# Kernel optimization log

Hardware: AMD Instinct MI355X
Metric: run time of the kernel (lower is better)

Reference implementation:

```python
import jax, jax.numpy as jnp
import numpy as np
from jax import lax

B, IC, OC, H, W_DIM, K = 8, 64, 64, 256, 512, 3
BLUR_1D = [1.0, 3.0, 3.0, 1.0]
FACTOR = 2
GAIN = 1.0


def _blur_kernel():
    # setup_resample_kernel: outer product of 1D kernel, normalized to sum 1
    k = np.asarray(BLUR_1D, dtype=np.float32)
    k = np.outer(k, k)
    k = k / np.sum(k)
    return k  # [4,4]


def setup_inputs() -> dict:
    key = jax.random.key(0)
    ks = jax.random.split(key, 5)
    x = jax.random.normal(ks[0], (B, IC, H, H), dtype=jnp.float32)
    w = jax.random.normal(ks[1], (B, W_DIM), dtype=jnp.float32)
    # init_std = 1.0 for both weights since lrmul = 1.0
    w_conv = jax.random.normal(ks[2], (K, K, IC, OC), dtype=jnp.float32)
    w_dense = jax.random.normal(ks[3], (W_DIM, IC), dtype=jnp.float32)
    b_mod = jnp.zeros((IC,), dtype=jnp.float32)
    return {"x": x, "w": w, "w_conv": w_conv, "w_dense": w_dense, "b_mod": b_mod}


def reference(x, w, w_conv, w_dense, b_mod):
    k = w_conv.shape[0]
    ic, oc = w_conv.shape[2], w_conv.shape[3]

    # runtime coefs (equalized lr): he_std = gain / sqrt(fan_in), lrmul = 1
    coef_conv = 1.0 / np.sqrt(k * k * ic)
    coef_dense = 1.0 / np.sqrt(w.shape[1])

    # style = Dense(w) + bias (linear act, gain 1) + 1.0   -> [B, IC]
    style = w @ (coef_dense * w_dense) + b_mod + 1.0

    # modulate: [B,k,k,IC,OC]
    wmod = (coef_conv * w_conv)[None] * style[:, None, None, :, None]
    # demodulate over (kh, kw, ic)
    d = lax.rsqrt(jnp.sum(jnp.square(wmod), axis=(1, 2, 3)) + 1e-8)  # [B,OC]
    wmod = wmod * d[:, None, None, None, :]

    # per-sample grouped transposed conv (upsample x2) == lhs-dilated cross-corr
    # with the unflipped modulated weight, padding k-1 on each side.
    w_oihw = jnp.transpose(wmod, (0, 4, 3, 1, 2))  # [B,OC,IC,k,k]

    def up_conv(xb, wb):
        return lax.conv_general_dilated(
            xb[None], wb, window_strides=(1, 1),
            padding=[(k - 1, k - 1), (k - 1, k - 1)],
            lhs_dilation=(FACTOR, FACTOR),
            dimension_numbers=("NCHW", "OIHW", "NCHW"))[0]

    y = jax.vmap(up_conv)(x, w_oihw)  # [B,OC,(H-1)*2+k,(W-1)*2+k] = [B,OC,513,513]

    # upfirdn blur: kernel scaled by gain * factor**2, pad0 = pad1 = 1,
    # true convolution (kernel flipped in reference) applied depthwise.
    kb = jnp.asarray(_blur_kernel() * (GAIN * FACTOR ** 2))  # [4,4]
    fw = kb[::-1, ::-1][None, None]  # [1,1,4,4]
    b_, c_, s1, s2 = y.shape
    y = lax.conv_general_dilated(
        y.reshape(b_ * c_, 1, s1, s2), fw, window_strides=(1, 1),
        padding=[(1, 1), (1, 1)],
        dimension_numbers=("NCHW", "OIHW", "NCHW"))
    # output spatial: s1 + 2 - 4 + 1 = 2H
    return y.reshape(b_, c_, y.shape[2], y.shape[3])
```

## Files before the change

kernel.cpp:

```cpp
#include <hip/hip_runtime.h>

#define NB 8
#define IC 64
#define OC 64
#define HH 256
#define WD 512
#define PP 258

typedef __bf16 bf16x8 __attribute__((ext_vector_type(8)));
typedef float f32x16 __attribute__((ext_vector_type(16)));
typedef float f32x4 __attribute__((ext_vector_type(4)));

__device__ inline void compute_E(const float* __restrict__ w_conv, float stv,
                                 int oc, float E[6][6]) {
  const float coef_conv = 1.0f / 24.0f;
  const float s = stv * coef_conv;
  const int ic = threadIdx.x & 63;

  float wm[3][3];
  float ssq = 0.f;
  #pragma unroll
  for (int kh = 0; kh < 3; ++kh)
    #pragma unroll
    for (int kw = 0; kw < 3; ++kw) {
      float v = w_conv[((kh * 3 + kw) * IC + ic) * OC + oc] * s;
      wm[kh][kw] = v;
      ssq += v * v;
    }
  #pragma unroll
  for (int off = 32; off > 0; off >>= 1) ssq += __shfl_xor(ssq, off);
  const float d = rsqrtf(ssq + 1e-8f);
  #pragma unroll
  for (int kh = 0; kh < 3; ++kh)
    #pragma unroll
    for (int kw = 0; kw < 3; ++kw) wm[kh][kw] *= d;

  const float g[4] = {0.25f, 0.75f, 0.75f, 0.25f};
  #pragma unroll
  for (int a = 0; a < 6; ++a)
    #pragma unroll
    for (int c = 0; c < 6; ++c) {
      float acc = 0.f;
      #pragma unroll
      for (int dh = 0; dh < 3; ++dh) {
        int u = a - dh;
        if (u < 0 || u > 3) continue;
        #pragma unroll
        for (int dw = 0; dw < 3; ++dw) {
          int v = c - dw;
          if (v < 0 || v > 3) continue;
          acc = fmaf(wm[dh][dw], g[u] * g[v], acc);
        }
      }
      E[a][c] = acc;
    }
}

__device__ inline float style_of(const float* __restrict__ w,
                                 const float* __restrict__ w_dense,
                                 const float* __restrict__ b_mod, int b,
                                 int ic) {
  const float coef_dense = 0.044194173824159216f;
  const float* wr = w + b * WD;
  float acc = 0.f;
  for (int k = 0; k < WD; ++k) acc = fmaf(wr[k], w_dense[k * IC + ic], acc);
  return acc * coef_dense + b_mod[ic] + 1.0f;
}

#define XS 268
__global__ __launch_bounds__(256) void pre_kernel(
    const float* __restrict__ x, const float* __restrict__ w,
    const float* __restrict__ w_dense, const float* __restrict__ b_mod,
    const float* __restrict__ w_conv, __bf16* __restrict__ xTg,
    __bf16* __restrict__ PWf) {
  __shared__ unsigned short buf[64 * XS];
  const int tid = threadIdx.x;
  const int bid = blockIdx.x;

  if (bid >= 2056) {
    const int bid2 = bid - 2056;
    const int b = bid2 >> 4;
    const int ocq = bid2 & 15;
    const int oc = ocq * 4 + (tid >> 6);
    const int ic = tid & 63;

    float stv = style_of(w, w_dense, b_mod, b, ic);
    float E[6][6];
    compute_E(w_conv, stv, oc, E);

    const int ks = ic >> 4;
    const int h = (ic >> 3) & 1;
    const int e = ic & 7;
    const int lane = (oc & 31) + 32 * h;
    const int ocg = oc >> 5;

    #pragma unroll
    for (int pp = 0; pp < 2; ++pp)
      #pragma unroll
      for (int pq = 0; pq < 2; ++pq) {
        const int ph = pp * 2 + pq;
        #pragma unroll
        for (int j = 0; j < 3; ++j)
          #pragma unroll
          for (int l = 0; l < 3; ++l) {
            const int tap = j * 3 + l;
            float val = E[2 * j + 1 - pp][2 * l + 1 - pq];
            size_t off =
                ((size_t)(((((b * 4 + ph) * 9 + tap) * 2 + ocg) * 4 + ks)) *
                     64 + lane) * 8 + e;
            PWf[off] = (__bf16)val;
          }
      }
    return;
  }

  const int m = bid % 257;
  const int b = bid / 257;

  if (m == 256) {
    uint4 z = make_uint4(0, 0, 0, 0);
    for (int i = tid; i < 8224; i += 256) {
      int pix = i >> 3;
      int sub = i & 7;
      int pr, pc;
      if (pix < 258) {
        pr = 0; pc = pix;
      } else if (pix < 516) {
        pr = 257; pc = pix - 258;
      } else {
        int rem = pix - 516;
        pr = 1 + (rem >> 1);
        pc = (rem & 1) ? 257 : 0;
      }
      *(uint4*)(xTg + ((size_t)(b * PP + pr) * PP + pc) * 64 + sub * 8) = z;
    }
    return;
  }

  const int ln = tid & 63, grp = tid >> 6;
  #pragma unroll
  for (int p = 0; p < 16; ++p) {
    const int ic = p * 4 + grp;
    float4 v = *(const float4*)(x + ((size_t)(b * 64 + ic) * 256 + m) * 256 +
                                ln * 4);
    ushort4 u4;
    u4.x = __builtin_bit_cast(unsigned short, (__bf16)v.x);
    u4.y = __builtin_bit_cast(unsigned short, (__bf16)v.y);
    u4.z = __builtin_bit_cast(unsigned short, (__bf16)v.z);
    u4.w = __builtin_bit_cast(unsigned short, (__bf16)v.w);
    *(ushort4*)&buf[ic * XS + ln * 4] = u4;
  }
  __syncthreads();
  #pragma unroll
  for (int it = 0; it < 8; ++it) {
    int pix = it * 32 + (tid >> 3);
    int g = tid & 7;
    bf16x8 o;
    #pragma unroll
    for (int e = 0; e < 8; ++e)
      o[e] = __builtin_bit_cast(__bf16, buf[(g * 8 + e) * XS + pix]);
    *(bf16x8*)(xTg + ((size_t)(b * PP + m + 1) * PP + (pix + 1)) * 64 +
               g * 8) = o;
  }
}

#define GLD_LDS(src, dst)                                                \
  __builtin_amdgcn_global_load_lds(                                      \
      (const __attribute__((address_space(1))) void*)(src),              \
      (__attribute__((address_space(3))) void*)(dst), 16, 0, 0)

__global__ __launch_bounds__(512, 2) void conv32f_kernel(
    const __bf16* __restrict__ xTg, const __bf16* __restrict__ PWf,
    float* __restrict__ out) {
  __shared__ __bf16 band[4 * 130 * 8 * 8];

  const int tid = threadIdx.x;
  const int lane = tid & 63;
  const int wv = tid >> 6;
  const int pq = wv & 1;
  const int pp = (wv >> 1) & 1;
  const int og = wv >> 2;
  const int ln31 = lane & 31;
  const int lh = lane >> 5;

  const int raw = blockIdx.x;
  const int bid = (raw & 7) * 256 + (raw >> 3);
  const int nh = bid & 1;
  const int mt = (bid >> 1) & 127;
  const int b = bid >> 8;
  const int mr = mt * 2;

  const int ph = b * 4 + pp * 2 + pq;
  const bf16x8* Awave =
      (const bf16x8*)PWf + ((size_t)ph * 72 + og * 4) * 64 + lane;

  {
    const int wb = wv * 520;
    #pragma unroll
    for (int it = 0; it < 9; ++it) {
      int o = it * 64 + lane;
      if (o < 520) {
        int L = wb + o;
        int row = L / 1040;
        int rem = L - row * 1040;
        int col = rem >> 3;
        int s = rem & 7;
        int g = s ^ (col & 7);
        const __bf16* src =
            xTg + ((size_t)(b * PP + mr + row) * PP + nh * 128 + col) * 64 +
            g * 8;
        GLD_LDS(src, band + (size_t)L * 8);
      }
    }
  }
  asm volatile("s_waitcnt vmcnt(0)" ::: "memory");
  __builtin_amdgcn_s_barrier();

  f32x16 acc[2][4];
  #pragma unroll
  for (int mw = 0; mw < 2; ++mw)
    #pragma unroll
    for (int ns = 0; ns < 4; ++ns)
      #pragma unroll
      for (int e = 0; e < 16; ++e) acc[mw][ns][e] = 0.f;

  #pragma unroll
  for (int ks = 0; ks < 4; ++ks) {
    #pragma unroll
    for (int l = 0; l < 3; ++l) {
      bf16x8 Ac[3];
      #pragma unroll
      for (int j = 0; j < 3; ++j) Ac[j] = Awave[((j * 3 + l) * 8 + ks) * 64];

      #pragma unroll
      for (int ns = 0; ns < 4; ++ns) {
        const int cc = ns * 32 + ln31 + l;
        const int slot = (ks * 2 + lh) ^ (cc & 7);
        bf16x8 Bf[4];
        #pragma unroll
        for (int r = 0; r < 4; ++r)
          Bf[r] = *(const bf16x8*)(band + ((size_t)((r * 130 + cc) * 8 +
                                                    slot)) * 8);
        __builtin_amdgcn_s_setprio(1);
        #pragma unroll
        for (int r = 0; r < 4; ++r) {
          #pragma unroll
          for (int j = 0; j < 3; ++j) {
            const int mw = r - j;
            if (mw == 0 || mw == 1) {
              acc[mw][ns] = __builtin_amdgcn_mfma_f32_32x32x16_bf16(
                  Ac[j], Bf[r], acc[mw][ns], 0, 0, 0);
            }
          }
        }
        __builtin_amdgcn_s_setprio(0);
      }
    }
  }

  __builtin_amdgcn_s_barrier();
  float* fb = (float*)band;
  const int pid = wv >> 1;

  #pragma unroll
  for (int mw = 0; mw < 2; ++mw) {
    #pragma unroll
    for (int eg = 0; eg < 4; ++eg) {
      #pragma unroll
      for (int i = 0; i < 4; ++i) {
        const int e = eg * 4 + i;
        const int ocb = i + 4 * lh;
        #pragma unroll
        for (int ns = 0; ns < 4; ++ns) {
          fb[(pid * 8 + ocb) * 260 + ns * 64 + 2 * ln31 + pq] =
              acc[mw][ns][e];
        }
      }
      __builtin_amdgcn_s_barrier();
      #pragma unroll
      for (int rro = 0; rro < 4; ++rro) {
        const int row = wv * 4 + rro;
        const int pid2 = row >> 3;
        const int ocb2 = row & 7;
        const int og2 = pid2 >> 1;
        const int pp2 = pid2 & 1;
        const int oc = og2 * 32 + (ocb2 & 3) + 8 * eg + 4 * (ocb2 >> 2);
        const int p = 2 * (mr + mw) + pp2;
        f32x4 v = *(const f32x4*)&fb[row * 260 + lane * 4];
        *(f32x4*)(out + ((size_t)(b * 64 + oc) * 512 + p) * 512 + nh * 256 +
                  lane * 4) = v;
      }
      __builtin_amdgcn_s_barrier();
    }
  }
}

__global__ __launch_bounds__(64) void pw_kernel(
    const float* __restrict__ w, const float* __restrict__ w_dense,
    const float* __restrict__ b_mod, const float* __restrict__ w_conv,
    float* __restrict__ PW) {
  const int oc = blockIdx.x;
  const int b = blockIdx.y;
  const int ic = threadIdx.x;
  float stv = style_of(w, w_dense, b_mod, b, ic);
  float E[6][6];
  compute_E(w_conv, stv, oc, E);
  #pragma unroll
  for (int pp = 0; pp < 2; ++pp)
    #pragma unroll
    for (int pq = 0; pq < 2; ++pq)
      #pragma unroll
      for (int j = 0; j < 3; ++j)
        #pragma unroll
        for (int l = 0; l < 3; ++l)
          PW[(((size_t)((b * 4 + pp * 2 + pq) * OC + oc) * IC + ic) * 9) +
             j * 3 + l] = E[2 * j + 1 - pp][2 * l + 1 - pq];
}

#define MT 16
#define NT 64
#define ICC 8
#define XROWS 18
#define XCOLS 66
#define XSTRIDE 68

__global__ __launch_bounds__(256) void conv_kernel(
    const float* __restrict__ x, const float* __restrict__ PW,
    float* __restrict__ out) {
  __shared__ float lds_x[ICC][XROWS][XSTRIDE];
  __shared__ float lds_w[4][ICC][9][4];

  const int tid = threadIdx.x;
  const int tn = tid & 15;
  const int tm = tid >> 4;
  const int bx = blockIdx.x;
  const int ntile = bx & 3;
  const int mtile = bx >> 2;
  const int ocg = blockIdx.y;
  const int b = blockIdx.z;
  const int m0 = mtile * MT;
  const int n0 = ntile * NT;

  float acc[4][4][4];
  #pragma unroll
  for (int o = 0; o < 4; ++o)
    #pragma unroll
    for (int ph = 0; ph < 4; ++ph)
      #pragma unroll
      for (int s = 0; s < 4; ++s) acc[o][ph][s] = 0.f;

  for (int ic0 = 0; ic0 < IC; ic0 += ICC) {
    __syncthreads();
    for (int ici = 0; ici < ICC; ++ici) {
      const float* xsrc = x + (size_t)(b * IC + ic0 + ici) * HH * HH;
      for (int rc = tid; rc < XROWS * XCOLS; rc += 256) {
        int r = rc / XCOLS;
        int c = rc - r * XCOLS;
        int gr = m0 - 1 + r;
        int gc = n0 - 1 + c;
        float v = 0.f;
        if ((unsigned)gr < HH && (unsigned)gc < HH) v = xsrc[gr * HH + gc];
        lds_x[ici][r][c] = v;
      }
    }
    for (int idx = tid; idx < 4 * ICC * 9 * 4; idx += 256) {
      int o = idx / (ICC * 9 * 4);
      int rem = idx - o * (ICC * 9 * 4);
      int ici = rem / 36;
      int r2 = rem - ici * 36;
      int t = r2 >> 2;
      int ph = r2 & 3;
      lds_w[o][ici][t][ph] =
          PW[(((size_t)((b * 4 + ph) * OC + (ocg * 4 + o)) * IC +
               (ic0 + ici)) * 9) + t];
    }
    __syncthreads();
    for (int ici = 0; ici < ICC; ++ici) {
      #pragma unroll
      for (int j = 0; j < 3; ++j) {
        const float* xr = &lds_x[ici][tm + j][tn * 4];
        float4 a4 = *(const float4*)xr;
        float2 a2 = *(const float2*)(xr + 4);
        float xv[6] = {a4.x, a4.y, a4.z, a4.w, a2.x, a2.y};
        #pragma unroll
        for (int l = 0; l < 3; ++l) {
          #pragma unroll
          for (int o = 0; o < 4; ++o) {
            float4 wv = *(const float4*)&lds_w[o][ici][j * 3 + l][0];
            #pragma unroll
            for (int s = 0; s < 4; ++s) {
              acc[o][0][s] = fmaf(wv.x, xv[l + s], acc[o][0][s]);
              acc[o][1][s] = fmaf(wv.y, xv[l + s], acc[o][1][s]);
              acc[o][2][s] = fmaf(wv.z, xv[l + s], acc[o][2][s]);
              acc[o][3][s] = fmaf(wv.w, xv[l + s], acc[o][3][s]);
            }
          }
        }
      }
    }
  }

  #pragma unroll
  for (int o = 0; o < 4; ++o) {
    #pragma unroll
    for (int pp = 0; pp < 2; ++pp) {
      const int p = 2 * (m0 + tm) + pp;
      float* dst = out +
          (((size_t)(b * OC + ocg * 4 + o) * 512 + p) * 512) + 2 * n0 + 8 * tn;
      float4 v0 = make_float4(acc[o][pp * 2 + 0][0], acc[o][pp * 2 + 1][0],
                              acc[o][pp * 2 + 0][1], acc[o][pp * 2 + 1][1]);
      float4 v1 = make_float4(acc[o][pp * 2 + 0][2], acc[o][pp * 2 + 1][2],
                              acc[o][pp * 2 + 0][3], acc[o][pp * 2 + 1][3]);
      *(float4*)dst = v0;
      *(float4*)(dst + 4) = v1;
    }
  }
}

extern "C" void kernel_launch(void* const* d_in, const int* in_sizes, int n_in,
                              void* d_out, int out_size, void* d_ws,
                              size_t ws_size, hipStream_t stream) {
  const float* x = (const float*)d_in[0];
  const float* w = (const float*)d_in[1];
  const float* w_conv = (const float*)d_in[2];
  const float* w_dense = (const float*)d_in[3];
  const float* b_mod = (const float*)d_in[4];
  float* out = (float*)d_out;

  const size_t PWF_BYTES = (size_t)8 * 4 * 9 * 2 * 4 * 64 * 8 * 2;
  const size_t XTG_BYTES = (size_t)8 * PP * PP * 64 * 2;
  const size_t NEED_NEW = PWF_BYTES + XTG_BYTES;

  if (ws_size >= NEED_NEW) {
    __bf16* PWf = (__bf16*)d_ws;
    __bf16* xTg = (__bf16*)((char*)d_ws + PWF_BYTES);
    pre_kernel<<<dim3(2056 + 128), 256, 0, stream>>>(x, w, w_dense, b_mod,
                                                     w_conv, xTg, PWf);
    conv32f_kernel<<<dim3(2048), 512, 0, stream>>>(xTg, PWf, out);
  } else {
    float* PW = (float*)d_ws;
    pw_kernel<<<dim3(OC, NB), 64, 0, stream>>>(w, w_dense, b_mod, w_conv, PW);
    conv_kernel<<<dim3(64, 16, NB), 256, 0, stream>>>(x, PW, out);
  }
}
```

Before: 250.3 us.

## Fuse input bf16 transpose/padding into conv kernel band load

Drops the pre-pass that converted x to a padded channel-last bf16 tensor in workspace. The conv kernel now reads fp32 x directly, converts it to bf16 and scatters it into the swizzled LDS band, with zero padding handled in-kernel. The modulated-weight precompute moves to its own small kernel. This removes a full write and re-read of the intermediate tensor. In exchange the band fill becomes scalar LDS stores with an extended swizzle, and overlapping halos are re-read from global memory by neighbouring tiles.

```diff
diff --git a/kernel.cpp b/kernel.cpp
--- a/kernel.cpp
+++ b/kernel.cpp
@@ -5,7 +5,6 @@
 #define OC 64
 #define HH 256
 #define WD 512
-#define PP 258
 
 typedef __bf16 bf16x8 __attribute__((ext_vector_type(8)));
 typedef float f32x16 __attribute__((ext_vector_type(16)));
@@ -67,110 +66,45 @@
   return acc * coef_dense + b_mod[ic] + 1.0f;
 }
 
-#define XS 268
-__global__ __launch_bounds__(256) void pre_kernel(
-    const float* __restrict__ x, const float* __restrict__ w,
-    const float* __restrict__ w_dense, const float* __restrict__ b_mod,
-    const float* __restrict__ w_conv, __bf16* __restrict__ xTg,
+__global__ __launch_bounds__(64) void pwfs_kernel(
+    const float* __restrict__ w, const float* __restrict__ w_dense,
+    const float* __restrict__ b_mod, const float* __restrict__ w_conv,
     __bf16* __restrict__ PWf) {
-  __shared__ unsigned short buf[64 * XS];
-  const int tid = threadIdx.x;
-  const int bid = blockIdx.x;
-
-  if (bid >= 2056) {
-    const int bid2 = bid - 2056;
-    const int b = bid2 >> 4;
-    const int ocq = bid2 & 15;
-    const int oc = ocq * 4 + (tid >> 6);
-    const int ic = tid & 63;
-
-    float stv = style_of(w, w_dense, b_mod, b, ic);
-    float E[6][6];
-    compute_E(w_conv, stv, oc, E);
-
-    const int ks = ic >> 4;
-    const int h = (ic >> 3) & 1;
-    const int e = ic & 7;
-    const int lane = (oc & 31) + 32 * h;
-    const int ocg = oc >> 5;
-
-    #pragma unroll
-    for (int pp = 0; pp < 2; ++pp)
-      #pragma unroll
-      for (int pq = 0; pq < 2; ++pq) {
-        const int ph = pp * 2 + pq;
-        #pragma unroll
-        for (int j = 0; j < 3; ++j)
-          #pragma unroll
-          for (int l = 0; l < 3; ++l) {
-            const int tap = j * 3 + l;
-            float val = E[2 * j + 1 - pp][2 * l + 1 - pq];
-            size_t off =
-                ((size_t)(((((b * 4 + ph) * 9 + tap) * 2 + ocg) * 4 + ks)) *
-                     64 + lane) * 8 + e;
-            PWf[off] = (__bf16)val;
-          }
-      }
-    return;
-  }
-
-  const int m = bid % 257;
-  const int b = bid / 257;
-
-  if (m == 256) {
-    uint4 z = make_uint4(0, 0, 0, 0);
-    for (int i = tid; i < 8224; i += 256) {
-      int pix = i >> 3;
-      int sub = i & 7;
-      int pr, pc;
-      if (pix < 258) {
-        pr = 0; pc = pix;
-      } else if (pix < 516) {
-        pr = 257; pc = pix - 258;
-      } else {
-        int rem = pix - 516;
-        pr = 1 + (rem >> 1);
-        pc = (rem & 1) ? 257 : 0;
-      }
-      *(uint4*)(xTg + ((size_t)(b * PP + pr) * PP + pc) * 64 + sub * 8) = z;
-    }
-    return;
-  }
-
-  const int ln = tid & 63, grp = tid >> 6;
-  #pragma unroll
-  for (int p = 0; p < 16; ++p) {
-    const int ic = p * 4 + grp;
-    float4 v = *(const float4*)(x + ((size_t)(b * 64 + ic) * 256 + m) * 256 +
-                                ln * 4);
-    ushort4 u4;
-    u4.x = __builtin_bit_cast(unsigned short, (__bf16)v.x);
-    u4.y = __builtin_bit_cast(unsigned short, (__bf16)v.y);
-    u4.z = __builtin_bit_cast(unsigned short, (__bf16)v.z);
-    u4.w = __builtin_bit_cast(unsigned short, (__bf16)v.w);
-    *(ushort4*)&buf[ic * XS + ln * 4] = u4;
-  }
-  __syncthreads();
-  #pragma unroll
-  for (int it = 0; it < 8; ++it) {
-    int pix = it * 32 + (tid >> 3);
-    int g = tid & 7;
-    bf16x8 o;
-    #pragma unroll
-    for (int e = 0; e < 8; ++e)
-      o[e] = __builtin_bit_cast(__bf16, buf[(g * 8 + e) * XS + pix]);
-    *(bf16x8*)(xTg + ((size_t)(b * PP + m + 1) * PP + (pix + 1)) * 64 +
-               g * 8) = o;
-  }
-}
-
-#define GLD_LDS(src, dst)                                                \
-  __builtin_amdgcn_global_load_lds(                                      \
-      (const __attribute__((address_space(1))) void*)(src),              \
-      (__attribute__((address_space(3))) void*)(dst), 16, 0, 0)
-
-__global__ __launch_bounds__(512, 2) void conv32f_kernel(
-    const __bf16* __restrict__ xTg, const __bf16* __restrict__ PWf,
+  const int oc = blockIdx.x;
+  const int b = blockIdx.y;
+  const int ic = threadIdx.x;
+
+  float stv = style_of(w, w_dense, b_mod, b, ic);
+  float E[6][6];
+  compute_E(w_conv, stv, oc, E);
+
+  const int ks = ic >> 4;
+  const int h = (ic >> 3) & 1;
+  const int e = ic & 7;
+  const int lane = (oc & 31) + 32 * h;
+  const int ocg = oc >> 5;
+
+  #pragma unroll
+  for (int pp = 0; pp < 2; ++pp)
+    #pragma unroll
+    for (int pq = 0; pq < 2; ++pq) {
+      const int ph = pp * 2 + pq;
+      #pragma unroll
+      for (int j = 0; j < 3; ++j)
+        #pragma unroll
+        for (int l = 0; l < 3; ++l) {
+          const int tap = j * 3 + l;
+          float val = E[2 * j + 1 - pp][2 * l + 1 - pq];
+          size_t off =
+              ((size_t)(((((b * 4 + ph) * 9 + tap) * 2 + ocg) * 4 + ks)) * 64 +
+               lane) * 8 + e;
+          PWf[off] = (__bf16)val;
+        }
+    }
+}
+
+__global__ __launch_bounds__(512, 2) void convf_kernel(
+    const float* __restrict__ x, const __bf16* __restrict__ PWf,
     float* __restrict__ out) {
   __shared__ __bf16 band[4 * 130 * 8 * 8];
 
@@ -195,26 +129,32 @@
       (const bf16x8*)PWf + ((size_t)ph * 72 + og * 4) * 64 + lane;
 
   {
-    const int wb = wv * 520;
-    #pragma unroll
-    for (int it = 0; it < 9; ++it) {
-      int o = it * 64 + lane;
-      if (o < 520) {
-        int L = wb + o;
-        int row = L / 1040;
-        int rem = L - row * 1040;
-        int col = rem >> 3;
-        int s = rem & 7;
-        int g = s ^ (col & 7);
-        const __bf16* src =
-            xTg + ((size_t)(b * PP + mr + row) * PP + nh * 128 + col) * 64 +
-            g * 8;
-        GLD_LDS(src, band + (size_t)L * 8);
-      }
-    }
-  }
-  asm volatile("s_waitcnt vmcnt(0)" ::: "memory");
-  __builtin_amdgcn_s_barrier();
+    const int laneC0 = nh * 128 - 4 + lane * 4;
+    const bool colOk = (lane < 34) && (laneC0 >= 0) && (laneC0 <= 252);
+    #pragma unroll 1
+    for (int it = 0; it < 32; ++it) {
+      const int task = wv * 32 + it;
+      const int ic = task & 63;
+      const int row = task >> 6;
+      const int R = mr - 1 + row;
+      float4 v = make_float4(0.f, 0.f, 0.f, 0.f);
+      if (colOk && (unsigned)R < 256u)
+        v = *(const float4*)(x + ((size_t)(b * 64 + ic) * 256 + R) * 256 +
+                             laneC0);
+      const int g = ic >> 3;
+      const int icb = ic & 7;
+      const float vv[4] = {v.x, v.y, v.z, v.w};
+      #pragma unroll
+      for (int k = 0; k < 4; ++k) {
+        const int c = lane * 4 + k - 3;
+        if ((unsigned)c <= 129u) {
+          const int slot = g ^ (c & 7) ^ ((c >> 3) & 7);
+          band[(((row * 130 + c) * 8 + slot) << 3) + icb] = (__bf16)vv[k];
+        }
+      }
+    }
+  }
+  __syncthreads();
 
   f32x16 acc[2][4];
   #pragma unroll
@@ -235,12 +175,12 @@
       #pragma unroll
       for (int ns = 0; ns < 4; ++ns) {
         const int cc = ns * 32 + ln31 + l;
-        const int slot = (ks * 2 + lh) ^ (cc & 7);
+        const int slot = (ks * 2 + lh) ^ (cc & 7) ^ ((cc >> 3) & 7);
         bf16x8 Bf[4];
         #pragma unroll
         for (int r = 0; r < 4; ++r)
-          Bf[r] = *(const bf16x8*)(band + ((size_t)((r * 130 + cc) * 8 +
-                                                    slot)) * 8);
+          Bf[r] = *(const bf16x8*)(band +
+                                   ((size_t)((r * 130 + cc) * 8 + slot)) * 8);
         __builtin_amdgcn_s_setprio(1);
         #pragma unroll
         for (int r = 0; r < 4; ++r) {
@@ -428,15 +368,12 @@
   float* out = (float*)d_out;
 
   const size_t PWF_BYTES = (size_t)8 * 4 * 9 * 2 * 4 * 64 * 8 * 2;
-  const size_t XTG_BYTES = (size_t)8 * PP * PP * 64 * 2;
-  const size_t NEED_NEW = PWF_BYTES + XTG_BYTES;
-
-  if (ws_size >= NEED_NEW) {
+
+  if (ws_size >= PWF_BYTES) {
     __bf16* PWf = (__bf16*)d_ws;
-    __bf16* xTg = (__bf16*)((char*)d_ws + PWF_BYTES);
-    pre_kernel<<<dim3(2056 + 128), 256, 0, stream>>>(x, w, w_dense, b_mod,
-                                                     w_conv, xTg, PWf);
-    conv32f_kernel<<<dim3(2048), 512, 0, stream>>>(xTg, PWf, out);
+    pwfs_kernel<<<dim3(OC, NB), 64, 0, stream>>>(w, w_dense, b_mod, w_conv,
+                                                 PWf);
+    convf_kernel<<<dim3(2048), 512, 0, stream>>>(x, PWf, out);
   } else {
     float* PW = (float*)d_ws;
     pw_kernel<<<dim3(OC, NB), 64, 0, stream>>>(w, w_dense, b_mod, w_conv, PW);
```

Result: slower. 364.6 us (+45.7%).

## Loop conv blocks over column tiles with double-buffered LDS staging and register-resident weights

Applied to the files above, without the earlier changes.

Each block now covers a full row pair and walks four 64-column tiles. The next tile's input band is prefetched into a second LDS buffer while the current one is computed and stored, and the grid is halved to match. All modulated weight fragments for the wave are loaded into registers once, instead of being re-read from global memory inside the k-loop. The aim is to hide the band-load latency and cut the repeated weight loads. The cost is heavy register pressure (36 bf16x8 fragments plus accumulators under a 512-thread, 2-blocks-per-CU bound), which risks spills or lower occupancy. There are also more barriers per block.

```diff
diff --git a/kernel.cpp b/kernel.cpp
--- a/kernel.cpp
+++ b/kernel.cpp
@@ -169,10 +169,11 @@
       (const __attribute__((address_space(1))) void*)(src),              \
       (__attribute__((address_space(3))) void*)(dst), 16, 0, 0)
 
-__global__ __launch_bounds__(512, 2) void conv32f_kernel(
+__global__ __launch_bounds__(512, 2) void convp_kernel(
     const __bf16* __restrict__ xTg, const __bf16* __restrict__ PWf,
     float* __restrict__ out) {
-  __shared__ __bf16 band[4 * 130 * 8 * 8];
+  __shared__ __bf16 band[2 * 2112 * 8];
+  __shared__ float fb[64 * 132];
 
   const int tid = threadIdx.x;
   const int lane = tid & 63;
@@ -182,114 +183,128 @@
   const int og = wv >> 2;
   const int ln31 = lane & 31;
   const int lh = lane >> 5;
+  const int pid = wv >> 1;
 
   const int raw = blockIdx.x;
-  const int bid = (raw & 7) * 256 + (raw >> 3);
-  const int nh = bid & 1;
-  const int mt = (bid >> 1) & 127;
-  const int b = bid >> 8;
+  const int bid = (raw & 7) * 128 + (raw >> 3);
+  const int mt = bid & 127;
+  const int b = bid >> 7;
   const int mr = mt * 2;
 
   const int ph = b * 4 + pp * 2 + pq;
   const bf16x8* Awave =
       (const bf16x8*)PWf + ((size_t)ph * 72 + og * 4) * 64 + lane;
 
-  {
-    const int wb = wv * 520;
-    #pragma unroll
-    for (int it = 0; it < 9; ++it) {
-      int o = it * 64 + lane;
-      if (o < 520) {
-        int L = wb + o;
-        int row = L / 1040;
-        int rem = L - row * 1040;
-        int col = rem >> 3;
-        int s = rem & 7;
-        int g = s ^ (col & 7);
+  bf16x8 A[9][4];
+  #pragma unroll
+  for (int tap = 0; tap < 9; ++tap)
+    #pragma unroll
+    for (int ks = 0; ks < 4; ++ks) A[tap][ks] = Awave[(tap * 8 + ks) * 64];
+
+  auto stage = [&](int t, int buf) {
+    #pragma unroll
+    for (int it = 0; it < 5; ++it) {
+      int idx = it * 512 + tid;
+      if (idx < 2112) {
+        int slot = idx & 7;
+        int pix = idx >> 3;
+        int row = pix / 66;
+        int c = pix - row * 66;
+        int g = slot ^ (c & 7);
         const __bf16* src =
-            xTg + ((size_t)(b * PP + mr + row) * PP + nh * 128 + col) * 64 +
+            xTg + ((size_t)(b * PP + mr + row) * PP + (t * 64 + c)) * 64 +
             g * 8;
-        GLD_LDS(src, band + (size_t)L * 8);
-      }
-    }
-  }
+        GLD_LDS(src, band + ((size_t)buf * 2112 + idx) * 8);
+      }
+    }
+  };
+
+  stage(0, 0);
   asm volatile("s_waitcnt vmcnt(0)" ::: "memory");
   __builtin_amdgcn_s_barrier();
 
-  f32x16 acc[2][4];
-  #pragma unroll
-  for (int mw = 0; mw < 2; ++mw)
-    #pragma unroll
-    for (int ns = 0; ns < 4; ++ns)
-      #pragma unroll
-      for (int e = 0; e < 16; ++e) acc[mw][ns][e] = 0.f;
-
-  #pragma unroll
-  for (int ks = 0; ks < 4; ++ks) {
-    #pragma unroll
-    for (int l = 0; l < 3; ++l) {
-      bf16x8 Ac[3];
-      #pragma unroll
-      for (int j = 0; j < 3; ++j) Ac[j] = Awave[((j * 3 + l) * 8 + ks) * 64];
-
-      #pragma unroll
-      for (int ns = 0; ns < 4; ++ns) {
-        const int cc = ns * 32 + ln31 + l;
-        const int slot = (ks * 2 + lh) ^ (cc & 7);
-        bf16x8 Bf[4];
-        #pragma unroll
-        for (int r = 0; r < 4; ++r)
-          Bf[r] = *(const bf16x8*)(band + ((size_t)((r * 130 + cc) * 8 +
+  #pragma unroll 1
+  for (int t = 0; t < 4; ++t) {
+    const int cur = t & 1;
+    if (t < 3) stage(t + 1, cur ^ 1);
+
+    const __bf16* bb = band + (size_t)cur * 2112 * 8;
+
+    f32x16 acc[2][2];
+    #pragma unroll
+    for (int mw = 0; mw < 2; ++mw)
+      #pragma unroll
+      for (int ns = 0; ns < 2; ++ns)
+        #pragma unroll
+        for (int e = 0; e < 16; ++e) acc[mw][ns][e] = 0.f;
+
+    #pragma unroll
+    for (int ks = 0; ks < 4; ++ks) {
+      #pragma unroll
+      for (int l = 0; l < 3; ++l) {
+        #pragma unroll
+        for (int ns = 0; ns < 2; ++ns) {
+          const int cc = ns * 32 + ln31 + l;
+          const int slot = (ks * 2 + lh) ^ (cc & 7);
+          bf16x8 Bf[4];
+          #pragma unroll
+          for (int r = 0; r < 4; ++r)
+            Bf[r] = *(const bf16x8*)(bb + ((size_t)((r * 66 + cc) * 8 +
                                                     slot)) * 8);
-        __builtin_amdgcn_s_setprio(1);
-        #pragma unroll
-        for (int r = 0; r < 4; ++r) {
+          __builtin_amdgcn_s_setprio(1);
           #pragma unroll
-          for (int j = 0; j < 3; ++j) {
-            const int mw = r - j;
-            if (mw == 0 || mw == 1) {
-              acc[mw][ns] = __builtin_amdgcn_mfma_f32_32x32x16_bf16(
-                  Ac[j], Bf[r], acc[mw][ns], 0, 0, 0);
+          for (int r = 0; r < 4; ++r) {
+            #pragma unroll
+            for (int j = 0; j < 3; ++j) {
+              const int mw = r - j;
+              if (mw == 0 || mw == 1) {
+                acc[mw][ns] = __builtin_amdgcn_mfma_f32_32x32x16_bf16(
+                    A[j * 3 + l][ks], Bf[r], acc[mw][ns], 0, 0, 0);
+              }
             }
           }
+          __builtin_amdgcn_s_setprio(0);
         }
-        __builtin_amdgcn_s_setprio(0);
-      }
-    }
-  }
-
-  __builtin_amdgcn_s_barrier();
-  float* fb = (float*)band;
-  const int pid = wv >> 1;
-
-  #pragma unroll
-  for (int mw = 0; mw < 2; ++mw) {
-    #pragma unroll
-    for (int eg = 0; eg < 4; ++eg) {
-      #pragma unroll
-      for (int i = 0; i < 4; ++i) {
-        const int e = eg * 4 + i;
-        const int ocb = i + 4 * lh;
-        #pragma unroll
-        for (int ns = 0; ns < 4; ++ns) {
-          fb[(pid * 8 + ocb) * 260 + ns * 64 + 2 * ln31 + pq] =
-              acc[mw][ns][e];
+      }
+    }
+
+    #pragma unroll
+    for (int r4 = 0; r4 < 4; ++r4) {
+      const int mw = r4 >> 1;
+      const int eh = r4 & 1;
+      #pragma unroll
+      for (int sub = 0; sub < 2; ++sub) {
+        #pragma unroll
+        for (int i = 0; i < 4; ++i) {
+          const int e = (eh * 2 + sub) * 4 + i;
+          const int fbrow = pid * 8 + (i + 4 * lh) + 32 * sub;
+          #pragma unroll
+          for (int ns = 0; ns < 2; ++ns)
+            fb[fbrow * 132 + ns * 64 + 2 * ln31 + pq] = acc[mw][ns][e];
         }
       }
       __builtin_amdgcn_s_barrier();
       #pragma unroll
-      for (int rro = 0; rro < 4; ++rro) {
-        const int row = wv * 4 + rro;
-        const int pid2 = row >> 3;
-        const int ocb2 = row & 7;
-        const int og2 = pid2 >> 1;
-        const int pp2 = pid2 & 1;
-        const int oc = og2 * 32 + (ocb2 & 3) + 8 * eg + 4 * (ocb2 >> 2);
-        const int p = 2 * (mr + mw) + pp2;
-        f32x4 v = *(const f32x4*)&fb[row * 260 + lane * 4];
-        *(f32x4*)(out + ((size_t)(b * 64 + oc) * 512 + p) * 512 + nh * 256 +
-                  lane * 4) = v;
-      }
+      for (int i2 = 0; i2 < 4; ++i2) {
+        const int row = wv * 8 + i2 * 2 + lh;
+        const int sub = row >> 5;
+        const int r5 = row & 31;
+        const int pid2 = r5 >> 3;
+        const int ocb2 = r5 & 7;
+        const int eg2 = eh * 2 + sub;
+        const int oc =
+            (pid2 >> 1) * 32 + (ocb2 & 3) + 8 * eg2 + 4 * (ocb2 >> 2);
+        const int p = 2 * (mr + mw) + (pid2 & 1);
+        const int col = ln31 * 4;
+        f32x4 v = *(const f32x4*)&fb[row * 132 + col];
+        *(f32x4*)(out + ((size_t)(b * 64 + oc) * 512 + p) * 512 + t * 128 +
+                  col) = v;
+      }
+      __builtin_amdgcn_s_barrier();
+    }
+
+    if (t < 3) {
+      asm volatile("s_waitcnt vmcnt(16)" ::: "memory");
       __builtin_amdgcn_s_barrier();
     }
   }
@@ -436,7 +451,7 @@
     __bf16* xTg = (__bf16*)((char*)d_ws + PWF_BYTES);
     pre_kernel<<<dim3(2056 + 128), 256, 0, stream>>>(x, w, w_dense, b_mod,
                                                      w_conv, xTg, PWf);
-    conv32f_kernel<<<dim3(2048), 512, 0, stream>>>(xTg, PWf, out);
+    convp_kernel<<<dim3(1024), 512, 0, stream>>>(xTg, PWf, out);
   } else {
     float* PW = (float*)d_ws;
     pw_kernel<<<dim3(OC, NB), 64, 0, stream>>>(w, w_dense, b_mod, w_conv, PW);
```

New measurement: 296.6 us. +18.5%, slower.
